# Kernel optimization log

Measured on AMD Instinct MI355X. Metric: run time of the kernel, lower is better.

Reference implementation:

```python
import math
import jax, jax.numpy as jnp
import numpy as np

N_NODES = 50000
N_EDGES = 800000
F_IN = 512
HID = 64
N_CLS = 64
NITER = 10


def setup_inputs() -> dict:
    key = jax.random.key(0)
    k = jax.random.split(key, 6)
    x = jax.random.normal(k[0], (N_NODES, F_IN), jnp.float32)
    edge_index = jax.random.randint(k[1], (2, N_EDGES), 0, N_NODES, jnp.int64)
    W1 = jax.random.normal(k[2], (F_IN, HID), jnp.float32) / np.sqrt(F_IN)
    b1 = jnp.zeros((HID,), jnp.float32)
    W2 = jax.random.normal(k[3], (HID, N_CLS), jnp.float32) / np.sqrt(HID)
    b2 = jnp.zeros((N_CLS,), jnp.float32)
    halt_w = jax.random.normal(k[4], (N_CLS,), jnp.float32) / np.sqrt(N_CLS)
    # reset_parameters: bias = log((1/(niter+1)) / (1 - 1/(niter+1)))
    b = math.log((1.0 / (NITER + 1)) / (1.0 - 1.0 / (NITER + 1)))
    halt_b = jnp.full((1,), b, jnp.float32)
    return {"x": x, "edge_index": edge_index, "W1": W1, "b1": b1,
            "W2": W2, "b2": b2, "halt_w": halt_w, "halt_b": halt_b}


def reference(x, edge_index, W1, b1, W2, b2, halt_w, halt_b):
    N = x.shape[0]
    # MLP (eval mode: dropout is identity)
    h = jnp.maximum(x @ W1 + b1, 0.0)
    local = h @ W2 + b2                      # [N, C] local predictions
    # GCN normalization with self-loops (eval: no edge dropout)
    loops = jnp.arange(N, dtype=edge_index.dtype)
    row = jnp.concatenate([edge_index[0], loops])
    col = jnp.concatenate([edge_index[1], loops])
    deg = jnp.zeros((N,), x.dtype).at[row].add(1.0)
    dis = jnp.where(deg > 0, jax.lax.rsqrt(jnp.maximum(deg, 1.0)), 0.0)
    norm = dis[row] * dis[col]               # [E+N]

    def step(carry, _):
        prop, steps, sum_h, cont, xacc = carry
        old = prop
        msg = norm[:, None] * prop[row]                       # gather + scale
        prop = jax.ops.segment_sum(msg, col, num_segments=N)  # scatter-add
        hh = jax.nn.sigmoid(prop @ halt_w + halt_b[0])        # [N]
        prob = (sum_h + hh < 0.99) & cont
        pf = prob.astype(x.dtype)
        steps = steps + pf
        sum_h = sum_h + pf * hh
        cond = prob & (steps < NITER)
        p = jnp.where(cond, sum_h, 1.0 - sum_h)
        xacc = xacc + (prop * p[:, None] + old * (1.0 - p)[:, None]) * cont.astype(x.dtype)[:, None]
        cont = cont & prob
        return (prop, steps, sum_h, cont, xacc), None

    init = (local, jnp.ones((N,), x.dtype), jnp.zeros((N,), x.dtype),
            jnp.ones((N,), bool), jnp.zeros_like(local))
    (prop, steps, sum_h, cont, xacc), _ = jax.lax.scan(step, init, None, length=NITER)
    out = xacc / steps[:, None]
    return jax.nn.log_softmax(out, axis=1), steps, 1.0 - sum_h
```

## Files before the change

kernel.cpp:

```cpp
#include <hip/hip_runtime.h>
#include <hip/hip_bf16.h>

#define F_IN 512
#define NC 64
#define NITER 10
#define BM 128

__global__ __launch_bounds__(256) void init_state_kernel(
    float* __restrict__ steps, float* __restrict__ sumh, int* __restrict__ cont,
    int N) {
  int i = blockIdx.x * blockDim.x + threadIdx.x;
  if (i < N) { steps[i] = 1.0f; sumh[i] = 0.0f; cont[i] = 1; }
}

__global__ __launch_bounds__(128) void mlp_kernel(
    const float* __restrict__ x, const float* __restrict__ W1,
    const float* __restrict__ b1, const float* __restrict__ W2,
    const float* __restrict__ b2, float* __restrict__ out, int N) {
  __shared__ float xs[BM * NC];
  __shared__ float ws[NC * NC];
  const int tid  = threadIdx.x;
  const int brow = blockIdx.x * BM;
  const int rg = tid >> 3;
  const int cg = tid & 7;
  const int r0 = rg * 8;
  const int c0 = cg * 8;
  const int keyr = rg & 7;

  float acc[8][8];
#pragma unroll
  for (int j = 0; j < 8; ++j) {
    float bv = b1[c0 + j];
#pragma unroll
    for (int i = 0; i < 8; ++i) acc[i][j] = bv;
  }

  for (int kt = 0; kt < F_IN; kt += 64) {
#pragma unroll
    for (int q = 0; q < 16; ++q) {
      int c = q * 128 + tid;
      int row = c >> 4, kc = c & 15;
      int gr = brow + row; if (gr >= N) gr = N - 1;
      float4 v = *reinterpret_cast<const float4*>(&x[(size_t)gr * F_IN + kt + kc * 4]);
      *reinterpret_cast<float4*>(&xs[row * NC + ((kc ^ ((row >> 3) & 7)) << 2)]) = v;
    }
#pragma unroll
    for (int q = 0; q < 8; ++q) {
      int c = q * 128 + tid;
      *reinterpret_cast<float4*>(&ws[c * 4]) =
          *reinterpret_cast<const float4*>(&W1[(size_t)kt * NC + c * 4]);
    }
    __syncthreads();
#pragma unroll 4
    for (int kc = 0; kc < 16; ++kc) {
      float xv[8][4];
#pragma unroll
      for (int i = 0; i < 8; ++i) {
        float4 t = *reinterpret_cast<const float4*>(
            &xs[(r0 + i) * NC + ((kc ^ keyr) << 2)]);
        xv[i][0] = t.x; xv[i][1] = t.y; xv[i][2] = t.z; xv[i][3] = t.w;
      }
#pragma unroll
      for (int m = 0; m < 4; ++m) {
        float4 wa = *reinterpret_cast<const float4*>(&ws[(kc * 4 + m) * NC + c0]);
        float4 wb = *reinterpret_cast<const float4*>(&ws[(kc * 4 + m) * NC + c0 + 4]);
        float wr[8] = {wa.x, wa.y, wa.z, wa.w, wb.x, wb.y, wb.z, wb.w};
#pragma unroll
        for (int i = 0; i < 8; ++i)
#pragma unroll
          for (int j = 0; j < 8; ++j)
            acc[i][j] = fmaf(xv[i][m], wr[j], acc[i][j]);
      }
    }
    __syncthreads();
  }

#pragma unroll
  for (int i = 0; i < 8; ++i) {
    float4 ha = make_float4(fmaxf(acc[i][0], 0.f), fmaxf(acc[i][1], 0.f),
                            fmaxf(acc[i][2], 0.f), fmaxf(acc[i][3], 0.f));
    float4 hb = make_float4(fmaxf(acc[i][4], 0.f), fmaxf(acc[i][5], 0.f),
                            fmaxf(acc[i][6], 0.f), fmaxf(acc[i][7], 0.f));
    *reinterpret_cast<float4*>(&xs[(r0 + i) * NC + (((cg * 2 + 0) ^ keyr) << 2)]) = ha;
    *reinterpret_cast<float4*>(&xs[(r0 + i) * NC + (((cg * 2 + 1) ^ keyr) << 2)]) = hb;
  }
#pragma unroll
  for (int q = 0; q < 8; ++q) {
    int c = q * 128 + tid;
    *reinterpret_cast<float4*>(&ws[c * 4]) =
        *reinterpret_cast<const float4*>(&W2[c * 4]);
  }
  float acc2[8][8];
#pragma unroll
  for (int j = 0; j < 8; ++j) {
    float bv = b2[c0 + j];
#pragma unroll
    for (int i = 0; i < 8; ++i) acc2[i][j] = bv;
  }
  __syncthreads();
#pragma unroll 4
  for (int kc = 0; kc < 16; ++kc) {
    float xv[8][4];
#pragma unroll
    for (int i = 0; i < 8; ++i) {
      float4 t = *reinterpret_cast<const float4*>(
          &xs[(r0 + i) * NC + ((kc ^ keyr) << 2)]);
      xv[i][0] = t.x; xv[i][1] = t.y; xv[i][2] = t.z; xv[i][3] = t.w;
    }
#pragma unroll
    for (int m = 0; m < 4; ++m) {
      float4 wa = *reinterpret_cast<const float4*>(&ws[(kc * 4 + m) * NC + c0]);
      float4 wb = *reinterpret_cast<const float4*>(&ws[(kc * 4 + m) * NC + c0 + 4]);
      float wr[8] = {wa.x, wa.y, wa.z, wa.w, wb.x, wb.y, wb.z, wb.w};
#pragma unroll
      for (int i = 0; i < 8; ++i)
#pragma unroll
        for (int j = 0; j < 8; ++j)
          acc2[i][j] = fmaf(xv[i][m], wr[j], acc2[i][j]);
    }
  }
#pragma unroll
  for (int i = 0; i < 8; ++i) {
    int gr = brow + r0 + i;
    if (gr < N) {
      float4 oa = make_float4(acc2[i][0], acc2[i][1], acc2[i][2], acc2[i][3]);
      float4 ob = make_float4(acc2[i][4], acc2[i][5], acc2[i][6], acc2[i][7]);
      *reinterpret_cast<float4*>(&out[(size_t)gr * NC + c0]) = oa;
      *reinterpret_cast<float4*>(&out[(size_t)gr * NC + c0 + 4]) = ob;
    }
  }
}

__global__ __launch_bounds__(256) void hist_kernel(
    const int* __restrict__ ei, int* __restrict__ deg_i,
    int* __restrict__ indeg, int E) {
  int e = blockIdx.x * blockDim.x + threadIdx.x;
  if (e < E) {
    atomicAdd(&deg_i[ei[e]], 1);
    atomicAdd(&indeg[ei[E + e]], 1);
  }
}

__global__ __launch_bounds__(256) void dis_kernel(
    const int* __restrict__ deg_i, float* __restrict__ dis, int N) {
  int i = blockIdx.x * blockDim.x + threadIdx.x;
  if (i < N) dis[i] = 1.0f / sqrtf((float)(deg_i[i] + 1));
}

__device__ __forceinline__ int pad8(int v) { return (v + 7) & ~7; }

__global__ __launch_bounds__(256) void scan_sum_kernel(
    const int* __restrict__ indeg, int* __restrict__ bsum, int N) {
  __shared__ int sm[256];
  int tid = threadIdx.x;
  int i = blockIdx.x * 256 + tid;
  sm[tid] = (i < N) ? pad8(indeg[i]) : 0;
  __syncthreads();
  for (int s = 128; s > 0; s >>= 1) {
    if (tid < s) sm[tid] += sm[tid + s];
    __syncthreads();
  }
  if (tid == 0) bsum[blockIdx.x] = sm[0];
}

__global__ __launch_bounds__(256) void scan_bsum_kernel(int* __restrict__ bsum, int nb) {
  __shared__ int sm[256];
  int tid = threadIdx.x;
  int v = (tid < nb) ? bsum[tid] : 0;
  sm[tid] = v;
  __syncthreads();
  for (int s = 1; s < 256; s <<= 1) {
    int t = (tid >= s) ? sm[tid - s] : 0;
    __syncthreads();
    sm[tid] += t;
    __syncthreads();
  }
  if (tid < nb) bsum[tid] = sm[tid] - v;
}

__global__ __launch_bounds__(256) void scan_final_kernel(
    const int* __restrict__ indeg, const int* __restrict__ bsum,
    int* __restrict__ rowptr, int N) {
  __shared__ int sm[256];
  int tid = threadIdx.x;
  int i = blockIdx.x * 256 + tid;
  int v = (i < N) ? pad8(indeg[i]) : 0;
  sm[tid] = v;
  __syncthreads();
  for (int s = 1; s < 256; s <<= 1) {
    int t = (tid >= s) ? sm[tid - s] : 0;
    __syncthreads();
    sm[tid] += t;
    __syncthreads();
  }
  if (i < N) {
    rowptr[i] = bsum[blockIdx.x] + sm[tid] - v;
    if (i == N - 1) rowptr[N] = bsum[blockIdx.x] + sm[tid];
  }
}

__global__ __launch_bounds__(256) void scatter_kernel(
    const int* __restrict__ ei, const int* __restrict__ rowptr,
    int* __restrict__ cursor, const float* __restrict__ dis,
    int2* __restrict__ csr, int E) {
  int e = blockIdx.x * blockDim.x + threadIdx.x;
  if (e < E) {
    int s = ei[e];
    int c = ei[E + e];
    int pos = rowptr[c] + atomicAdd(&cursor[c], 1);
    csr[pos] = make_int2(s, __float_as_int(dis[s] * dis[c]));
  }
}

__global__ __launch_bounds__(256) void prop_step_kernel(
    const float* __restrict__ prop, float* __restrict__ prop_new,
    const int2* __restrict__ csr, const int* __restrict__ rowptr,
    const float* __restrict__ dis, const float* __restrict__ hw,
    const float* __restrict__ hb, float* __restrict__ steps,
    float* __restrict__ sumh, int* __restrict__ cont,
    float* __restrict__ xacc, int N) {
  int wid = (int)((blockIdx.x * blockDim.x + threadIdx.x) >> 6);
  if (wid >= N) return;
  int lane = threadIdx.x & 63;
  size_t rowoff = (size_t)wid * NC + lane;

  float oldv = prop[rowoff];
  float dc = dis[wid];
  int beg = __builtin_amdgcn_readfirstlane(rowptr[wid]);
  int end = __builtin_amdgcn_readfirstlane(rowptr[wid + 1]);

  float a[8];
  a[0] = dc * dc * oldv;
#pragma unroll
  for (int u = 1; u < 8; ++u) a[u] = 0.0f;
  for (int i = beg; i < end; i += 8) {
    int2 e[8];
#pragma unroll
    for (int u = 0; u < 8; ++u) e[u] = csr[i + u];
#pragma unroll
    for (int u = 0; u < 8; ++u)
      a[u] = fmaf(__int_as_float(e[u].y), prop[(size_t)e[u].x * NC + lane], a[u]);
  }
  float acc = ((a[0] + a[1]) + (a[2] + a[3])) + ((a[4] + a[5]) + (a[6] + a[7]));
  prop_new[rowoff] = acc;

  float z = acc * hw[lane];
#pragma unroll
  for (int off = 32; off > 0; off >>= 1) z += __shfl_xor(z, off);
  z += hb[0];
  float hh = 1.0f / (1.0f + expf(-z));

  float st = steps[wid], sh = sumh[wid];
  int ct = cont[wid];
  bool prob = ((sh + hh) < 0.99f) && (ct != 0);
  float pf = prob ? 1.0f : 0.0f;
  st += pf;
  sh += pf * hh;
  bool cond = prob && (st < (float)NITER);
  float pp = cond ? sh : (1.0f - sh);
  float ctf = ct ? 1.0f : 0.0f;
  xacc[rowoff] += (acc * pp + oldv * (1.0f - pp)) * ctf;
  if (lane == 0) { steps[wid] = st; sumh[wid] = sh; cont[wid] = prob ? 1 : 0; }
}

__global__ __launch_bounds__(256) void final_kernel(
    const float* __restrict__ xacc, const float* __restrict__ steps,
    const float* __restrict__ sumh, float* __restrict__ out0,
    float* __restrict__ out1, float* __restrict__ out2, int N) {
  int wid = (int)((blockIdx.x * blockDim.x + threadIdx.x) >> 6);
  if (wid >= N) return;
  int lane = threadIdx.x & 63;
  float st = steps[wid];
  float v = xacc[(size_t)wid * NC + lane] / st;
  float m = v;
#pragma unroll
  for (int off = 32; off > 0; off >>= 1) m = fmaxf(m, __shfl_xor(m, off));
  float e = expf(v - m);
  float s = e;
#pragma unroll
  for (int off = 32; off > 0; off >>= 1) s += __shfl_xor(s, off);
  out0[(size_t)wid * NC + lane] = v - m - logf(s);
  if (lane == 0) { out1[wid] = st; out2[wid] = 1.0f - sumh[wid]; }
}

extern "C" void kernel_launch(void* const* d_in, const int* in_sizes, int n_in,
                              void* d_out, int out_size, void* d_ws, size_t ws_size,
                              hipStream_t stream) {
  const float* x      = (const float*)d_in[0];
  const int*   ei     = (const int*)d_in[1];
  const float* W1     = (const float*)d_in[2];
  const float* b1     = (const float*)d_in[3];
  const float* W2     = (const float*)d_in[4];
  const float* b2     = (const float*)d_in[5];
  const float* halt_w = (const float*)d_in[6];
  const float* halt_b = (const float*)d_in[7];

  const int N = in_sizes[0] / F_IN;
  const int E = in_sizes[1] / 2;
  const int EP = E + 8 * N;

  char* p = (char*)d_ws;
  auto alloc = [&](size_t bytes) {
    void* r = (void*)p;
    p += (bytes + 255) & ~(size_t)255;
    return r;
  };
  float* propA  = (float*)alloc((size_t)N * NC * 4);
  float* propB  = (float*)alloc((size_t)N * NC * 4);
  float* xacc   = (float*)alloc((size_t)N * NC * 4);
  int2*  csr    = (int2*)alloc((size_t)EP * 8);
  int*   rowptr = (int*)alloc((size_t)(N + 1) * 4);
  int*   deg_i  = (int*)alloc((size_t)N * 4);
  int*   indeg  = (int*)alloc((size_t)N * 4);
  int*   cursor = (int*)alloc((size_t)N * 4);
  float* dis    = (float*)alloc((size_t)N * 4);
  float* steps  = (float*)alloc((size_t)N * 4);
  float* sumh   = (float*)alloc((size_t)N * 4);
  int*   cont   = (int*)alloc((size_t)N * 4);
  int*   bsum   = (int*)alloc(1024);

  hipMemsetAsync(deg_i,  0, (size_t)N * 4, stream);
  hipMemsetAsync(indeg,  0, (size_t)N * 4, stream);
  hipMemsetAsync(cursor, 0, (size_t)N * 4, stream);
  hipMemsetAsync(xacc,   0, (size_t)N * NC * 4, stream);
  hipMemsetAsync(csr,    0, (size_t)EP * 8, stream);

  const int nbN = (N + 255) / 256;
  const int nbE = (E + 255) / 256;
  const int nbM = (N + BM - 1) / BM;

  init_state_kernel<<<nbN, 256, 0, stream>>>(steps, sumh, cont, N);
  mlp_kernel<<<nbM, 128, 0, stream>>>(x, W1, b1, W2, b2, propA, N);
  hist_kernel<<<nbE, 256, 0, stream>>>(ei, deg_i, indeg, E);
  dis_kernel<<<nbN, 256, 0, stream>>>(deg_i, dis, N);
  scan_sum_kernel<<<nbN, 256, 0, stream>>>(indeg, bsum, N);
  scan_bsum_kernel<<<1, 256, 0, stream>>>(bsum, nbN);
  scan_final_kernel<<<nbN, 256, 0, stream>>>(indeg, bsum, rowptr, N);
  scatter_kernel<<<nbE, 256, 0, stream>>>(ei, rowptr, cursor, dis, csr, E);

  float* out0 = (float*)d_out;
  float* out1 = out0 + (size_t)N * NC;
  float* out2 = out1 + N;

  const float* cur = propA;
  float* nxt = propB;
  const int nbW = (N + 3) / 4;
  for (int it = 0; it < NITER; ++it) {
    prop_step_kernel<<<nbW, 256, 0, stream>>>(cur, nxt, csr, rowptr, dis,
                                              halt_w, halt_b, steps, sumh,
                                              cont, xacc, N);
    const float* t = nxt; nxt = (float*)cur; cur = t;
  }
  final_kernel<<<nbW, 256, 0, stream>>>(xacc, steps, sumh, out0, out1, out2, N);
}
```

Measured before the change: 580.4 us.

## Fuse init/final into templated prop steps, retile MLP, drop big memsets

Folds state initialization into the first propagation step and the log-softmax finalization into the last step via template flags, removing two kernels and the xacc memset. Replaces the full CSR memset with a kernel that zeroes only padding slots, and merges the dis computation into the scan-sum kernel. The MLP kernel moves to 256 threads each computing an 8x4 tile, and nontemporal loads/stores are used for streaming CSR, xacc and output traffic. The changes trade fewer launches and less memset bandwidth for more template variants and a small serial padding loop per node.

```diff
diff --git a/kernel.cpp b/kernel.cpp
--- a/kernel.cpp
+++ b/kernel.cpp
@@ -6,14 +6,9 @@
 #define NITER 10
 #define BM 128
 
-__global__ __launch_bounds__(256) void init_state_kernel(
-    float* __restrict__ steps, float* __restrict__ sumh, int* __restrict__ cont,
-    int N) {
-  int i = blockIdx.x * blockDim.x + threadIdx.x;
-  if (i < N) { steps[i] = 1.0f; sumh[i] = 0.0f; cont[i] = 1; }
-}
-
-__global__ __launch_bounds__(128) void mlp_kernel(
+typedef float fvec4 __attribute__((ext_vector_type(4)));
+
+__global__ __launch_bounds__(256) void mlp_kernel(
     const float* __restrict__ x, const float* __restrict__ W1,
     const float* __restrict__ b1, const float* __restrict__ W2,
     const float* __restrict__ b2, float* __restrict__ out, int N) {
@@ -21,15 +16,15 @@
   __shared__ float ws[NC * NC];
   const int tid  = threadIdx.x;
   const int brow = blockIdx.x * BM;
-  const int rg = tid >> 3;
-  const int cg = tid & 7;
+  const int rg = tid >> 4;
+  const int cg = tid & 15;
   const int r0 = rg * 8;
-  const int c0 = cg * 8;
+  const int c0 = cg * 4;
   const int keyr = rg & 7;
 
-  float acc[8][8];
-#pragma unroll
-  for (int j = 0; j < 8; ++j) {
+  float acc[8][4];
+#pragma unroll
+  for (int j = 0; j < 4; ++j) {
     float bv = b1[c0 + j];
 #pragma unroll
     for (int i = 0; i < 8; ++i) acc[i][j] = bv;
@@ -37,62 +32,56 @@
 
   for (int kt = 0; kt < F_IN; kt += 64) {
 #pragma unroll
-    for (int q = 0; q < 16; ++q) {
-      int c = q * 128 + tid;
+    for (int q = 0; q < 8; ++q) {
+      int c = q * 256 + tid;
       int row = c >> 4, kc = c & 15;
       int gr = brow + row; if (gr >= N) gr = N - 1;
       float4 v = *reinterpret_cast<const float4*>(&x[(size_t)gr * F_IN + kt + kc * 4]);
       *reinterpret_cast<float4*>(&xs[row * NC + ((kc ^ ((row >> 3) & 7)) << 2)]) = v;
     }
 #pragma unroll
-    for (int q = 0; q < 8; ++q) {
-      int c = q * 128 + tid;
+    for (int q = 0; q < 4; ++q) {
+      int c = q * 256 + tid;
       *reinterpret_cast<float4*>(&ws[c * 4]) =
           *reinterpret_cast<const float4*>(&W1[(size_t)kt * NC + c * 4]);
     }
     __syncthreads();
 #pragma unroll 4
     for (int kc = 0; kc < 16; ++kc) {
-      float xv[8][4];
-#pragma unroll
-      for (int i = 0; i < 8; ++i) {
-        float4 t = *reinterpret_cast<const float4*>(
-            &xs[(r0 + i) * NC + ((kc ^ keyr) << 2)]);
-        xv[i][0] = t.x; xv[i][1] = t.y; xv[i][2] = t.z; xv[i][3] = t.w;
+      float4 xq[8];
+#pragma unroll
+      for (int i = 0; i < 8; ++i)
+        xq[i] = *reinterpret_cast<const float4*>(&xs[(r0 + i) * NC + ((kc ^ keyr) << 2)]);
+#pragma unroll
+      for (int m = 0; m < 4; ++m) {
+        float4 wv = *reinterpret_cast<const float4*>(&ws[(kc * 4 + m) * NC + c0]);
+        float wr[4] = {wv.x, wv.y, wv.z, wv.w};
+#pragma unroll
+        for (int i = 0; i < 8; ++i) {
+          float xm = reinterpret_cast<const float*>(&xq[i])[m];
+#pragma unroll
+          for (int j = 0; j < 4; ++j) acc[i][j] = fmaf(xm, wr[j], acc[i][j]);
+        }
       }
-#pragma unroll
-      for (int m = 0; m < 4; ++m) {
-        float4 wa = *reinterpret_cast<const float4*>(&ws[(kc * 4 + m) * NC + c0]);
-        float4 wb = *reinterpret_cast<const float4*>(&ws[(kc * 4 + m) * NC + c0 + 4]);
-        float wr[8] = {wa.x, wa.y, wa.z, wa.w, wb.x, wb.y, wb.z, wb.w};
-#pragma unroll
-        for (int i = 0; i < 8; ++i)
-#pragma unroll
-          for (int j = 0; j < 8; ++j)
-            acc[i][j] = fmaf(xv[i][m], wr[j], acc[i][j]);
-      }
     }
     __syncthreads();
   }
 
 #pragma unroll
   for (int i = 0; i < 8; ++i) {
-    float4 ha = make_float4(fmaxf(acc[i][0], 0.f), fmaxf(acc[i][1], 0.f),
+    float4 hv = make_float4(fmaxf(acc[i][0], 0.f), fmaxf(acc[i][1], 0.f),
                             fmaxf(acc[i][2], 0.f), fmaxf(acc[i][3], 0.f));
-    float4 hb = make_float4(fmaxf(acc[i][4], 0.f), fmaxf(acc[i][5], 0.f),
-                            fmaxf(acc[i][6], 0.f), fmaxf(acc[i][7], 0.f));
-    *reinterpret_cast<float4*>(&xs[(r0 + i) * NC + (((cg * 2 + 0) ^ keyr) << 2)]) = ha;
-    *reinterpret_cast<float4*>(&xs[(r0 + i) * NC + (((cg * 2 + 1) ^ keyr) << 2)]) = hb;
-  }
-#pragma unroll
-  for (int q = 0; q < 8; ++q) {
-    int c = q * 128 + tid;
+    *reinterpret_cast<float4*>(&xs[(r0 + i) * NC + ((cg ^ keyr) << 2)]) = hv;
+  }
+#pragma unroll
+  for (int q = 0; q < 4; ++q) {
+    int c = q * 256 + tid;
     *reinterpret_cast<float4*>(&ws[c * 4]) =
         *reinterpret_cast<const float4*>(&W2[c * 4]);
   }
-  float acc2[8][8];
-#pragma unroll
-  for (int j = 0; j < 8; ++j) {
+  float acc2[8][4];
+#pragma unroll
+  for (int j = 0; j < 4; ++j) {
     float bv = b2[c0 + j];
 #pragma unroll
     for (int i = 0; i < 8; ++i) acc2[i][j] = bv;
@@ -100,33 +89,28 @@
   __syncthreads();
 #pragma unroll 4
   for (int kc = 0; kc < 16; ++kc) {
-    float xv[8][4];
-#pragma unroll
-    for (int i = 0; i < 8; ++i) {
-      float4 t = *reinterpret_cast<const float4*>(
-          &xs[(r0 + i) * NC + ((kc ^ keyr) << 2)]);
-      xv[i][0] = t.x; xv[i][1] = t.y; xv[i][2] = t.z; xv[i][3] = t.w;
-    }
+    float4 xq[8];
+#pragma unroll
+    for (int i = 0; i < 8; ++i)
+      xq[i] = *reinterpret_cast<const float4*>(&xs[(r0 + i) * NC + ((kc ^ keyr) << 2)]);
 #pragma unroll
     for (int m = 0; m < 4; ++m) {
-      float4 wa = *reinterpret_cast<const float4*>(&ws[(kc * 4 + m) * NC + c0]);
-      float4 wb = *reinterpret_cast<const float4*>(&ws[(kc * 4 + m) * NC + c0 + 4]);
-      float wr[8] = {wa.x, wa.y, wa.z, wa.w, wb.x, wb.y, wb.z, wb.w};
-#pragma unroll
-      for (int i = 0; i < 8; ++i)
-#pragma unroll
-        for (int j = 0; j < 8; ++j)
-          acc2[i][j] = fmaf(xv[i][m], wr[j], acc2[i][j]);
+      float4 wv = *reinterpret_cast<const float4*>(&ws[(kc * 4 + m) * NC + c0]);
+      float wr[4] = {wv.x, wv.y, wv.z, wv.w};
+#pragma unroll
+      for (int i = 0; i < 8; ++i) {
+        float xm = reinterpret_cast<const float*>(&xq[i])[m];
+#pragma unroll
+        for (int j = 0; j < 4; ++j) acc2[i][j] = fmaf(xm, wr[j], acc2[i][j]);
+      }
     }
   }
 #pragma unroll
   for (int i = 0; i < 8; ++i) {
     int gr = brow + r0 + i;
     if (gr < N) {
-      float4 oa = make_float4(acc2[i][0], acc2[i][1], acc2[i][2], acc2[i][3]);
-      float4 ob = make_float4(acc2[i][4], acc2[i][5], acc2[i][6], acc2[i][7]);
-      *reinterpret_cast<float4*>(&out[(size_t)gr * NC + c0]) = oa;
-      *reinterpret_cast<float4*>(&out[(size_t)gr * NC + c0 + 4]) = ob;
+      fvec4 o = {acc2[i][0], acc2[i][1], acc2[i][2], acc2[i][3]};
+      __builtin_nontemporal_store(o, reinterpret_cast<fvec4*>(&out[(size_t)gr * NC + c0]));
     }
   }
 }
@@ -141,20 +125,16 @@
   }
 }
 
-__global__ __launch_bounds__(256) void dis_kernel(
+__device__ __forceinline__ int pad8(int v) { return (v + 7) & ~7; }
+
+__global__ __launch_bounds__(256) void scan_sum_kernel(
+    const int* __restrict__ indeg, int* __restrict__ bsum,
     const int* __restrict__ deg_i, float* __restrict__ dis, int N) {
-  int i = blockIdx.x * blockDim.x + threadIdx.x;
-  if (i < N) dis[i] = 1.0f / sqrtf((float)(deg_i[i] + 1));
-}
-
-__device__ __forceinline__ int pad8(int v) { return (v + 7) & ~7; }
-
-__global__ __launch_bounds__(256) void scan_sum_kernel(
-    const int* __restrict__ indeg, int* __restrict__ bsum, int N) {
   __shared__ int sm[256];
   int tid = threadIdx.x;
   int i = blockIdx.x * 256 + tid;
   sm[tid] = (i < N) ? pad8(indeg[i]) : 0;
+  if (i < N) dis[i] = 1.0f / sqrtf((float)(deg_i[i] + 1));
   __syncthreads();
   for (int s = 128; s > 0; s >>= 1) {
     if (tid < s) sm[tid] += sm[tid + s];
@@ -212,13 +192,26 @@
   }
 }
 
+__global__ __launch_bounds__(256) void pad_fill_kernel(
+    const int* __restrict__ rowptr, const int* __restrict__ indeg,
+    int2* __restrict__ csr, int N) {
+  int i = blockIdx.x * blockDim.x + threadIdx.x;
+  if (i < N) {
+    int e = rowptr[i] + indeg[i];
+    int end = rowptr[i + 1];
+    for (; e < end; ++e) csr[e] = make_int2(0, 0);
+  }
+}
+
+template<bool FIRST, bool LAST>
 __global__ __launch_bounds__(256) void prop_step_kernel(
     const float* __restrict__ prop, float* __restrict__ prop_new,
     const int2* __restrict__ csr, const int* __restrict__ rowptr,
     const float* __restrict__ dis, const float* __restrict__ hw,
     const float* __restrict__ hb, float* __restrict__ steps,
     float* __restrict__ sumh, int* __restrict__ cont,
-    float* __restrict__ xacc, int N) {
+    float* __restrict__ xacc, float* __restrict__ out0,
+    float* __restrict__ out1, float* __restrict__ out2, int N) {
   int wid = (int)((blockIdx.x * blockDim.x + threadIdx.x) >> 6);
   if (wid >= N) return;
   int lane = threadIdx.x & 63;
@@ -234,15 +227,20 @@
 #pragma unroll
   for (int u = 1; u < 8; ++u) a[u] = 0.0f;
   for (int i = beg; i < end; i += 8) {
-    int2 e[8];
-#pragma unroll
-    for (int u = 0; u < 8; ++u) e[u] = csr[i + u];
+    long long raw[8];
 #pragma unroll
     for (int u = 0; u < 8; ++u)
-      a[u] = fmaf(__int_as_float(e[u].y), prop[(size_t)e[u].x * NC + lane], a[u]);
+      raw[u] = __builtin_nontemporal_load(
+          reinterpret_cast<const long long*>(csr + i + u));
+#pragma unroll
+    for (int u = 0; u < 8; ++u) {
+      int src = (int)(raw[u] & 0xffffffffLL);
+      float w = __int_as_float((int)(raw[u] >> 32));
+      a[u] = fmaf(w, prop[(size_t)src * NC + lane], a[u]);
+    }
   }
   float acc = ((a[0] + a[1]) + (a[2] + a[3])) + ((a[4] + a[5]) + (a[6] + a[7]));
-  prop_new[rowoff] = acc;
+  if (!LAST) __builtin_nontemporal_store(acc, &prop_new[rowoff]);
 
   float z = acc * hw[lane];
 #pragma unroll
@@ -250,8 +248,9 @@
   z += hb[0];
   float hh = 1.0f / (1.0f + expf(-z));
 
-  float st = steps[wid], sh = sumh[wid];
-  int ct = cont[wid];
+  float st, sh; int ct;
+  if (FIRST) { st = 1.0f; sh = 0.0f; ct = 1; }
+  else { st = steps[wid]; sh = sumh[wid]; ct = cont[wid]; }
   bool prob = ((sh + hh) < 0.99f) && (ct != 0);
   float pf = prob ? 1.0f : 0.0f;
   st += pf;
@@ -259,28 +258,27 @@
   bool cond = prob && (st < (float)NITER);
   float pp = cond ? sh : (1.0f - sh);
   float ctf = ct ? 1.0f : 0.0f;
-  xacc[rowoff] += (acc * pp + oldv * (1.0f - pp)) * ctf;
-  if (lane == 0) { steps[wid] = st; sumh[wid] = sh; cont[wid] = prob ? 1 : 0; }
-}
-
-__global__ __launch_bounds__(256) void final_kernel(
-    const float* __restrict__ xacc, const float* __restrict__ steps,
-    const float* __restrict__ sumh, float* __restrict__ out0,
-    float* __restrict__ out1, float* __restrict__ out2, int N) {
-  int wid = (int)((blockIdx.x * blockDim.x + threadIdx.x) >> 6);
-  if (wid >= N) return;
-  int lane = threadIdx.x & 63;
-  float st = steps[wid];
-  float v = xacc[(size_t)wid * NC + lane] / st;
-  float m = v;
-#pragma unroll
-  for (int off = 32; off > 0; off >>= 1) m = fmaxf(m, __shfl_xor(m, off));
-  float e = expf(v - m);
-  float s = e;
-#pragma unroll
-  for (int off = 32; off > 0; off >>= 1) s += __shfl_xor(s, off);
-  out0[(size_t)wid * NC + lane] = v - m - logf(s);
-  if (lane == 0) { out1[wid] = st; out2[wid] = 1.0f - sumh[wid]; }
+  float xa = FIRST ? 0.0f : __builtin_nontemporal_load(&xacc[rowoff]);
+  float xnew = xa + (acc * pp + oldv * (1.0f - pp)) * ctf;
+
+  if (!LAST) {
+    __builtin_nontemporal_store(xnew, &xacc[rowoff]);
+    if (lane == 0) { steps[wid] = st; sumh[wid] = sh; cont[wid] = prob ? 1 : 0; }
+  } else {
+    float v = xnew / st;
+    float m = v;
+#pragma unroll
+    for (int off = 32; off > 0; off >>= 1) m = fmaxf(m, __shfl_xor(m, off));
+    float e = expf(v - m);
+    float s = e;
+#pragma unroll
+    for (int off = 32; off > 0; off >>= 1) s += __shfl_xor(s, off);
+    __builtin_nontemporal_store(v - m - logf(s), &out0[rowoff]);
+    if (lane == 0) {
+      __builtin_nontemporal_store(st, &out1[wid]);
+      __builtin_nontemporal_store(1.0f - sh, &out2[wid]);
+    }
+  }
 }
 
 extern "C" void kernel_launch(void* const* d_in, const int* in_sizes, int n_in,
@@ -322,34 +320,37 @@
   hipMemsetAsync(deg_i,  0, (size_t)N * 4, stream);
   hipMemsetAsync(indeg,  0, (size_t)N * 4, stream);
   hipMemsetAsync(cursor, 0, (size_t)N * 4, stream);
-  hipMemsetAsync(xacc,   0, (size_t)N * NC * 4, stream);
-  hipMemsetAsync(csr,    0, (size_t)EP * 8, stream);
 
   const int nbN = (N + 255) / 256;
   const int nbE = (E + 255) / 256;
   const int nbM = (N + BM - 1) / BM;
 
-  init_state_kernel<<<nbN, 256, 0, stream>>>(steps, sumh, cont, N);
-  mlp_kernel<<<nbM, 128, 0, stream>>>(x, W1, b1, W2, b2, propA, N);
+  mlp_kernel<<<nbM, 256, 0, stream>>>(x, W1, b1, W2, b2, propA, N);
   hist_kernel<<<nbE, 256, 0, stream>>>(ei, deg_i, indeg, E);
-  dis_kernel<<<nbN, 256, 0, stream>>>(deg_i, dis, N);
-  scan_sum_kernel<<<nbN, 256, 0, stream>>>(indeg, bsum, N);
+  scan_sum_kernel<<<nbN, 256, 0, stream>>>(indeg, bsum, deg_i, dis, N);
   scan_bsum_kernel<<<1, 256, 0, stream>>>(bsum, nbN);
   scan_final_kernel<<<nbN, 256, 0, stream>>>(indeg, bsum, rowptr, N);
   scatter_kernel<<<nbE, 256, 0, stream>>>(ei, rowptr, cursor, dis, csr, E);
+  pad_fill_kernel<<<nbN, 256, 0, stream>>>(rowptr, indeg, csr, N);
 
   float* out0 = (float*)d_out;
   float* out1 = out0 + (size_t)N * NC;
   float* out2 = out1 + N;
 
+  const int nbW = (N + 3) / 4;
   const float* cur = propA;
   float* nxt = propB;
-  const int nbW = (N + 3) / 4;
-  for (int it = 0; it < NITER; ++it) {
-    prop_step_kernel<<<nbW, 256, 0, stream>>>(cur, nxt, csr, rowptr, dis,
-                                              halt_w, halt_b, steps, sumh,
-                                              cont, xacc, N);
+  prop_step_kernel<true, false><<<nbW, 256, 0, stream>>>(
+      cur, nxt, csr, rowptr, dis, halt_w, halt_b, steps, sumh, cont, xacc,
+      out0, out1, out2, N);
+  { const float* t = nxt; nxt = (float*)cur; cur = t; }
+  for (int it = 1; it < NITER - 1; ++it) {
+    prop_step_kernel<false, false><<<nbW, 256, 0, stream>>>(
+        cur, nxt, csr, rowptr, dis, halt_w, halt_b, steps, sumh, cont, xacc,
+        out0, out1, out2, N);
     const float* t = nxt; nxt = (float*)cur; cur = t;
   }
-  final_kernel<<<nbW, 256, 0, stream>>>(xacc, steps, sumh, out0, out1, out2, N);
-}
+  prop_step_kernel<false, true><<<nbW, 256, 0, stream>>>(
+      cur, nxt, csr, rowptr, dis, halt_w, halt_b, steps, sumh, cont, xacc,
+      out0, out1, out2, N);
+}
```

Result: faster. 554.5 us (-4.5%).
